# Optimization experiments

Measured on AMD Instinct MI355X. Metric: run time of the kernel, lower is better.

The kernel has to match this reference:

```python
import jax, jax.numpy as jnp
import numpy as np

G, N, E, B = 4, 50000, 800000, 32
F_IN, H, HEADS, NUM_NODES = 64, 128, 8, 50000
HD = H // HEADS
LO, HI = 50.0, 110.0


def setup_inputs() -> dict:
    key = jax.random.key(0)
    ks = jax.random.split(key, 10)
    x = jax.random.normal(ks[0], (G, N, F_IN), jnp.float32)
    edge_index = jax.random.randint(ks[1], (G, 2, E), 0, N)
    batch = jnp.sort(jax.random.randint(ks[2], (G, N), 0, B), axis=-1)
    init = lambda k, shape, fan: (jax.random.normal(k, shape, jnp.float32) / np.sqrt(fan)).astype(jnp.float32)
    W1 = init(ks[3], (F_IN, H), F_IN); b1 = jnp.zeros((H,), jnp.float32)
    W2 = init(ks[4], (H, H), H);       b2 = jnp.zeros((H,), jnp.float32)
    in_proj_w = init(ks[5], (3 * H, H), H); in_proj_b = jnp.zeros((3 * H,), jnp.float32)
    out_proj_w = init(ks[6], (H, H), H);    out_proj_b = jnp.zeros((H,), jnp.float32)
    lin_w = init(ks[7], (NUM_NODES, H), H); lin_b = jnp.zeros((NUM_NODES,), jnp.float32)
    return dict(x=x, edge_index=edge_index, batch=batch, W1=W1, b1=b1, W2=W2, b2=b2,
                in_proj_w=in_proj_w, in_proj_b=in_proj_b, out_proj_w=out_proj_w,
                out_proj_b=out_proj_b, lin_w=lin_w, lin_b=lin_b)


def _gcn(x, row, col, W, b):
    # PyG GCNConv: add self-loops, sym-normalized scatter-add aggregation.
    h = x @ W  # [N,H]
    deg = jax.ops.segment_sum(jnp.ones((E,), x.dtype), col, num_segments=N) + 1.0  # +1 self-loop
    dinv = jax.lax.rsqrt(deg)
    norm = dinv[row] * dinv[col]  # [E]
    agg = jax.ops.segment_sum(h[row] * norm[:, None], col, num_segments=N)
    agg = agg + h * (1.0 / deg)[:, None]  # self-loop message (norm = 1/deg)
    return agg + b


def _per_graph(xg, eig, bg, W1, b1, W2, b2):
    row, col = eig[0], eig[1]
    h = jax.nn.relu(_gcn(xg, row, col, W1, b1))
    h = jax.nn.relu(_gcn(h, row, col, W2, b2))
    s = jax.ops.segment_sum(h, bg, num_segments=B)  # [B,H]
    cnt = jax.ops.segment_sum(jnp.ones((N,), h.dtype), bg, num_segments=B)
    return jnp.where(cnt[:, None] > 0, s / jnp.maximum(cnt, 1.0)[:, None], 0.0)


def reference(x, edge_index, batch, W1, b1, W2, b2, in_proj_w, in_proj_b,
              out_proj_w, out_proj_b, lin_w, lin_b):
    # per-graph GCN + mean pool -> embeddings [G, B, H] (seq-first for torch MHA)
    emb = jax.vmap(_per_graph, in_axes=(0, 0, 0, None, None, None, None))(
        x, edge_index, batch, W1, b1, W2, b2)
    # torch MultiheadAttention (self-attention, seq-first)
    q = emb @ in_proj_w[:H].T + in_proj_b[:H]
    k = emb @ in_proj_w[H:2 * H].T + in_proj_b[H:2 * H]
    v = emb @ in_proj_w[2 * H:].T + in_proj_b[2 * H:]
    qh = q.reshape(G, B, HEADS, HD)
    kh = k.reshape(G, B, HEADS, HD)
    vh = v.reshape(G, B, HEADS, HD)
    scores = jnp.einsum('gbhd,kbhd->bhgk', qh, kh) / np.sqrt(HD)
    attn = jax.nn.softmax(scores, axis=-1)
    ctx = jnp.einsum('bhgk,kbhd->gbhd', attn, vh).reshape(G, B, H)
    attended = ctx @ out_proj_w.T + out_proj_b  # [G,B,H]
    pooled = attended.mean(axis=1)  # [G,H]
    out = pooled @ lin_w.T + lin_b  # [G,NUM_NODES]
    return out * (HI - LO) + LO
```

## Files before the change

kernel.cpp:

```cpp
#include <hip/hip_runtime.h>

#define Gn 4
#define Nn 50000
#define En 800000
#define Bq 32
#define F_IN 64
#define Hn 128
#define NNODES 50000
#define NBK 196
#define EB 98

using v8s = __attribute__((ext_vector_type(8))) short;
using v4f = __attribute__((ext_vector_type(4))) float;

__device__ __forceinline__ float bf2f(unsigned short u) {
    unsigned int x = ((unsigned int)u) << 16;
    float f; __builtin_memcpy(&f, &x, 4); return f;
}
__device__ __forceinline__ unsigned short f2bf(float f) {
    unsigned int x; __builtin_memcpy(&x, &f, 4);
    x = (x + 0x7fffu + ((x >> 16) & 1u)) >> 16;
    return (unsigned short)x;
}

__global__ __launch_bounds__(256) void k_btot(const int* __restrict__ ei, int* __restrict__ btot,
                                              int* __restrict__ chist) {
    __shared__ int h[NBK];
    int g = blockIdx.y;
    const int* col = ei + (size_t)g * 2 * En + En;
    for (int i = threadIdx.x; i < NBK; i += 256) h[i] = 0;
    __syncthreads();
    int e0 = blockIdx.x * 8192, e1 = min(e0 + 8192, En);
    for (int i = e0 / 4 + threadIdx.x; i < e1 / 4; i += 256) {
        int4 c = ((const int4*)col)[i];
        atomicAdd(&h[c.x >> 8], 1);
        atomicAdd(&h[c.y >> 8], 1);
        atomicAdd(&h[c.z >> 8], 1);
        atomicAdd(&h[c.w >> 8], 1);
    }
    __syncthreads();
    int* ch = chist + ((size_t)g * EB + blockIdx.x) * NBK;
    for (int i = threadIdx.x; i < NBK; i += 256) {
        int v = h[i];
        ch[i] = v;
        if (v) atomicAdd(&btot[g * NBK + i], v);
    }
}

__global__ __launch_bounds__(256) void k_bbase(const int* __restrict__ btot, int* __restrict__ bbase,
                                               int* __restrict__ bcur) {
    __shared__ int s[256];
    int g = blockIdx.x, t = threadIdx.x;
    int v = (t < NBK) ? btot[g * NBK + t] : 0;
    s[t] = v;
    __syncthreads();
    for (int d = 1; d < 256; d <<= 1) {
        int u = (t >= d) ? s[t - d] : 0;
        __syncthreads();
        s[t] += u;
        __syncthreads();
    }
    if (t < NBK) { int b = s[t] - v; bbase[g * NBK + t] = b; bcur[g * NBK + t] = b; }
}

__global__ __launch_bounds__(256) void k_bucket(const int* __restrict__ ei, int* __restrict__ bcur,
                                                unsigned int* __restrict__ pairs,
                                                const int* __restrict__ chist) {
    __shared__ int h[NBK];
    __shared__ int gbase[NBK];
    int g = blockIdx.y;
    const int* row = ei + (size_t)g * 2 * En;
    const int* col = row + En;
    unsigned int* pg = pairs + (size_t)g * En;
    const int* ch = chist + ((size_t)g * EB + blockIdx.x) * NBK;
    for (int i = threadIdx.x; i < NBK; i += 256) {
        int cnt = ch[i];
        gbase[i] = cnt ? atomicAdd(&bcur[g * NBK + i], cnt) : 0;
        h[i] = 0;
    }
    __syncthreads();
    int e0 = blockIdx.x * 8192, e1 = min(e0 + 8192, En);
    for (int i = e0 / 4 + threadIdx.x; i < e1 / 4; i += 256) {
        int4 c = ((const int4*)col)[i];
        int4 r = ((const int4*)row)[i];
        int p;
        p = gbase[c.x >> 8] + atomicAdd(&h[c.x >> 8], 1); pg[p] = ((unsigned)r.x << 16) | (unsigned)c.x;
        p = gbase[c.y >> 8] + atomicAdd(&h[c.y >> 8], 1); pg[p] = ((unsigned)r.y << 16) | (unsigned)c.y;
        p = gbase[c.z >> 8] + atomicAdd(&h[c.z >> 8], 1); pg[p] = ((unsigned)r.z << 16) | (unsigned)c.z;
        p = gbase[c.w >> 8] + atomicAdd(&h[c.w >> 8], 1); pg[p] = ((unsigned)r.w << 16) | (unsigned)c.w;
    }
}

__global__ __launch_bounds__(256) void k_fillb2(const unsigned int* __restrict__ pairs,
                                                const int* __restrict__ bbase, const int* __restrict__ btot,
                                                int* __restrict__ off, float* __restrict__ dinv,
                                                unsigned short* __restrict__ srcs) {
    __shared__ int h[256], sc[256], curL[256];
    int g = blockIdx.y, b = blockIdx.x, t = threadIdx.x;
    int beg = bbase[g * NBK + b], cnt = btot[g * NBK + b];
    const unsigned int* pg = pairs + (size_t)g * En + beg;
    unsigned short* sg = srcs + (size_t)g * En;
    h[t] = 0;
    __syncthreads();
    for (int i = t; i < cnt; i += 256) atomicAdd(&h[pg[i] & 255], 1);
    __syncthreads();
    int d = h[t];
    sc[t] = d;
    __syncthreads();
    for (int dd = 1; dd < 256; dd <<= 1) {
        int u = (t >= dd) ? sc[t - dd] : 0;
        __syncthreads();
        sc[t] += u;
        __syncthreads();
    }
    int myoff = beg + sc[t] - d;
    int node = b * 256 + t;
    if (node < Nn) {
        off[g * (Nn + 1) + node] = myoff;
        dinv[g * Nn + node] = rsqrtf((float)d + 1.0f);
    }
    if (b == NBK - 1 && t == 255) off[g * (Nn + 1) + Nn] = beg + sc[255];
    curL[t] = myoff;
    __syncthreads();
    for (int i = t; i < cnt; i += 256) {
        unsigned int pr = pg[i];
        int pos = atomicAdd(&curL[pr & 255], 1);
        sg[pos] = (unsigned short)(pr >> 16);
    }
}

__global__ __launch_bounds__(256) void k_cast(const float* __restrict__ x, const float* __restrict__ dinv,
                                              unsigned short* __restrict__ xbs) {
    int g = blockIdx.y;
    int i = blockIdx.x * 256 + threadIdx.x;
    if (i >= Nn * 16) return;
    float dc = dinv[g * Nn + (i >> 4)];
    float4 v = *(const float4*)&x[(size_t)g * Nn * 64 + i * 4];
    ushort4 u = make_ushort4(f2bf(v.x * dc), f2bf(v.y * dc), f2bf(v.z * dc), f2bf(v.w * dc));
    *(ushort4*)&xbs[(size_t)g * Nn * 64 + i * 4] = u;
}

__global__ __launch_bounds__(256) void k_agg1(const unsigned short* __restrict__ xs_, const int* __restrict__ off_,
                                              const unsigned short* __restrict__ srcs_,
                                              const float* __restrict__ dinv_, unsigned short* __restrict__ z1_) {
    int g = blockIdx.y;
    const unsigned short* xs = xs_ + (size_t)g * Nn * 64;
    const int* off = off_ + g * (Nn + 1);
    const unsigned short* srcs = srcs_ + (size_t)g * En;
    unsigned short* z1 = z1_ + (size_t)g * Nn * 64;
    int node = blockIdx.x * 8 + (threadIdx.x >> 5);
    int lane = threadIdx.x & 31;
    int sub = lane >> 3;
    int fo = lane & 7;
    int beg = off[node], end = off[node + 1];
    int d = end - beg;
    int dm1 = max(d - 1, 0);
    int nst = (d + 3) >> 2;
    float acc[8] = {};
    int sb = srcs[beg + min(sub, dm1)];
    v8s c = *(const v8s*)&xs[(long)sb * 64 + fo * 8];
    sb = srcs[beg + min(4 + sub, dm1)];
    for (int st = 0; st < nst; ++st) {
        v8s n = *(const v8s*)&xs[(long)sb * 64 + fo * 8];
        sb = srcs[beg + min((st + 2) * 4 + sub, dm1)];
        float m = (st * 4 + sub < d) ? 1.f : 0.f;
#pragma unroll
        for (int q = 0; q < 8; ++q) acc[q] += m * bf2f((unsigned short)c[q]);
        c = n;
    }
#pragma unroll
    for (int q = 0; q < 8; ++q) {
        acc[q] += __shfl_xor(acc[q], 8, 32);
        acc[q] += __shfl_xor(acc[q], 16, 32);
    }
    if (sub == 0) {
        float dc = dinv_[g * Nn + node];
        v8s ow = *(const v8s*)&xs[(long)node * 64 + fo * 8];
        ushort4 o0, o1;
        o0.x = f2bf((acc[0] + bf2f((unsigned short)ow[0])) * dc);
        o0.y = f2bf((acc[1] + bf2f((unsigned short)ow[1])) * dc);
        o0.z = f2bf((acc[2] + bf2f((unsigned short)ow[2])) * dc);
        o0.w = f2bf((acc[3] + bf2f((unsigned short)ow[3])) * dc);
        o1.x = f2bf((acc[4] + bf2f((unsigned short)ow[4])) * dc);
        o1.y = f2bf((acc[5] + bf2f((unsigned short)ow[5])) * dc);
        o1.z = f2bf((acc[6] + bf2f((unsigned short)ow[6])) * dc);
        o1.w = f2bf((acc[7] + bf2f((unsigned short)ow[7])) * dc);
        *(ushort4*)&z1[(long)node * 64 + fo * 8] = o0;
        *(ushort4*)&z1[(long)node * 64 + fo * 8 + 4] = o1;
    }
}

__global__ __launch_bounds__(256) void k_agg2(const unsigned short* __restrict__ h_, const int* __restrict__ off_,
                                              const unsigned short* __restrict__ srcs_,
                                              const float* __restrict__ dinv_, unsigned short* __restrict__ z2_) {
    int g = blockIdx.y;
    const unsigned short* h = h_ + (size_t)g * Nn * 128;
    const int* off = off_ + g * (Nn + 1);
    const unsigned short* srcs = srcs_ + (size_t)g * En;
    unsigned short* z2 = z2_ + (size_t)g * Nn * 128;
    int node = blockIdx.x * 8 + (threadIdx.x >> 5);
    int lane = threadIdx.x & 31;
    int sub = lane >> 3;
    int fo = lane & 7;
    int beg = off[node], end = off[node + 1];
    int d = end - beg;
    int dm1 = max(d - 1, 0);
    int nst = (d + 3) >> 2;
    float acc[16] = {};
    int sb = srcs[beg + min(sub, dm1)];
    const unsigned short* rp = &h[(long)sb * 128 + fo * 16];
    v8s c0 = *(const v8s*)rp;
    v8s c1 = *(const v8s*)(rp + 8);
    sb = srcs[beg + min(4 + sub, dm1)];
    for (int st = 0; st < nst; ++st) {
        const unsigned short* rpn = &h[(long)sb * 128 + fo * 16];
        v8s n0 = *(const v8s*)rpn;
        v8s n1 = *(const v8s*)(rpn + 8);
        sb = srcs[beg + min((st + 2) * 4 + sub, dm1)];
        float m = (st * 4 + sub < d) ? 1.f : 0.f;
#pragma unroll
        for (int q = 0; q < 8; ++q) acc[q] += m * bf2f((unsigned short)c0[q]);
#pragma unroll
        for (int q = 0; q < 8; ++q) acc[8 + q] += m * bf2f((unsigned short)c1[q]);
        c0 = n0; c1 = n1;
    }
#pragma unroll
    for (int q = 0; q < 16; ++q) {
        acc[q] += __shfl_xor(acc[q], 8, 32);
        acc[q] += __shfl_xor(acc[q], 16, 32);
    }
    if (sub == 0) {
        float dc = dinv_[g * Nn + node];
        const unsigned short* op = &h[(long)node * 128 + fo * 16];
        unsigned short* zp = &z2[(long)node * 128 + fo * 16];
#pragma unroll
        for (int q4 = 0; q4 < 4; ++q4) {
            ushort4 ow = *(const ushort4*)(op + q4 * 4);
            ushort4 o;
            o.x = f2bf((acc[q4 * 4 + 0] + bf2f(ow.x)) * dc);
            o.y = f2bf((acc[q4 * 4 + 1] + bf2f(ow.y)) * dc);
            o.z = f2bf((acc[q4 * 4 + 2] + bf2f(ow.z)) * dc);
            o.w = f2bf((acc[q4 * 4 + 3] + bf2f(ow.w)) * dc);
            *(ushort4*)(zp + q4 * 4) = o;
        }
    }
}

template <int K, bool SCALE>
__global__ __launch_bounds__(256) void k_mmfma(const unsigned short* __restrict__ zin_,
                                               const float* __restrict__ W, const float* __restrict__ bias,
                                               const float* __restrict__ dinv_,
                                               unsigned short* __restrict__ outp_) {
    __shared__ __align__(16) unsigned short Wt[128 * (K + 8)];
    __shared__ __align__(16) unsigned short At[32 * (K + 8)];
    int g = blockIdx.y;
    const unsigned short* zin = zin_ + (size_t)g * Nn * K;
    const float* dinv = dinv_ + g * Nn;
    unsigned short* outp = outp_ + (size_t)g * Nn * 128;
    int t = threadIdx.x;
    int base = blockIdx.x * 32;

#pragma unroll
    for (int i = 0; i < K * 128 / 256; ++i) {
        int idx = i * 256 + t;
        int k = idx >> 7, n = idx & 127;
        Wt[n * (K + 8) + k] = f2bf(W[idx]);
    }
    {
        int r = t >> 3, cb = (t & 7) * (K / 8);
        long grow = base + r;
#pragma unroll
        for (int j = 0; j < K / 32; ++j) {
            ushort4 u = make_ushort4(0, 0, 0, 0);
            if (grow < Nn) u = *(const ushort4*)&zin[grow * K + cb + j * 4];
            *(ushort4*)&At[r * (K + 8) + cb + j * 4] = u;
        }
    }
    __syncthreads();

    int w = t >> 6, lane = t & 63;
    int wm = w & 1, wn = w >> 1;
    int m = lane & 15, q = lane >> 4;
    v4f acc[4] = {};
    const unsigned short* Ap = &At[(wm * 16 + m) * (K + 8) + q * 8];
    const unsigned short* Bp = &Wt[(wn * 64 + m) * (K + 8) + q * 8];
    const int rstep = 16 * (K + 8);
#pragma unroll
    for (int ks = 0; ks < K / 32; ++ks) {
        v8s a = *(const v8s*)(Ap + ks * 32);
        v8s b0 = *(const v8s*)(Bp + 0 * rstep + ks * 32);
        v8s b1 = *(const v8s*)(Bp + 1 * rstep + ks * 32);
        v8s b2 = *(const v8s*)(Bp + 2 * rstep + ks * 32);
        v8s b3 = *(const v8s*)(Bp + 3 * rstep + ks * 32);
        acc[0] = __builtin_amdgcn_mfma_f32_16x16x32_bf16(a, b0, acc[0], 0, 0, 0);
        acc[1] = __builtin_amdgcn_mfma_f32_16x16x32_bf16(a, b1, acc[1], 0, 0, 0);
        acc[2] = __builtin_amdgcn_mfma_f32_16x16x32_bf16(a, b2, acc[2], 0, 0, 0);
        acc[3] = __builtin_amdgcn_mfma_f32_16x16x32_bf16(a, b3, acc[3], 0, 0, 0);
    }

    int col0 = wn * 64 + m;
    int rbase = base + wm * 16 + q * 4;
    float dv[4];
#pragma unroll
    for (int rg = 0; rg < 4; ++rg)
        dv[rg] = SCALE ? ((rbase + rg < Nn) ? dinv[rbase + rg] : 1.f) : 1.f;
#pragma unroll
    for (int nt = 0; nt < 4; ++nt) {
        float bc = bias[col0 + nt * 16];
#pragma unroll
        for (int rg = 0; rg < 4; ++rg) {
            int row = rbase + rg;
            if (row < Nn) {
                float o = fmaxf(acc[nt][rg] + bc, 0.f);
                outp[(long)row * 128 + col0 + nt * 16] = f2bf(o * dv[rg]);
            }
        }
    }
}

__global__ __launch_bounds__(128) void k_pool(const unsigned short* __restrict__ y_, const int* __restrict__ bat,
                                              float* __restrict__ emb_sum, float* __restrict__ cnt) {
    int g = blockIdx.y;
    const unsigned short* y = y_ + (size_t)g * Nn * 128;
    const int* batch = bat + (size_t)g * Nn;
    int f = threadIdx.x;
    int start = blockIdx.x * 64;
    int end = min(start + 64, Nn);
    if (start >= Nn) return;
    float acc = 0.f;
    int cacc = 0;
    int cur = batch[start];
    for (int i = start; i < end; ++i) {
        int b = batch[i];
        if (b != cur) {
            atomicAdd(&emb_sum[(g * Bq + cur) * Hn + f], acc);
            if (f == 0) atomicAdd(&cnt[g * Bq + cur], (float)cacc);
            acc = 0.f; cacc = 0; cur = b;
        }
        acc += bf2f(y[(long)i * Hn + f]);
        cacc++;
    }
    atomicAdd(&emb_sum[(g * Bq + cur) * Hn + f], acc);
    if (f == 0) atomicAdd(&cnt[g * Bq + cur], (float)cacc);
}

__global__ __launch_bounds__(128) void k_attn(const float* __restrict__ emb_sum, const float* __restrict__ cnt,
                                              const float* __restrict__ ipw, const float* __restrict__ ipb,
                                              const float* __restrict__ opw, const float* __restrict__ opb,
                                              float* __restrict__ pooled) {
    int b = blockIdx.x;
    int f = threadIdx.x;
    __shared__ float es[4][128], qs[4][128], ks[4][128], vs[4][128], sc[128], cx[4][128];
#pragma unroll
    for (int g = 0; g < 4; ++g) {
        float c = cnt[g * Bq + b];
        es[g][f] = (c > 0.f) ? emb_sum[(g * Bq + b) * Hn + f] / c : 0.f;
    }
    __syncthreads();
#pragma unroll
    for (int g = 0; g < 4; ++g) {
        float q = ipb[f], k = ipb[Hn + f], v = ipb[2 * Hn + f];
        for (int j = 0; j < Hn; ++j) {
            float e = es[g][j];
            q += e * ipw[f * Hn + j];
            k += e * ipw[(Hn + f) * Hn + j];
            v += e * ipw[(2 * Hn + f) * Hn + j];
        }
        qs[g][f] = q; ks[g][f] = k; vs[g][f] = v;
    }
    __syncthreads();
    {
        int h = f >> 4, g = (f >> 2) & 3, kk = f & 3;
        float s = 0.f;
        for (int d = 0; d < 16; ++d) s += qs[g][h * 16 + d] * ks[kk][h * 16 + d];
        sc[f] = s * 0.25f;
    }
    __syncthreads();
    {
        int h = f >> 4;
#pragma unroll
        for (int g = 0; g < 4; ++g) {
            int bi = h * 16 + g * 4;
            float s0 = sc[bi], s1 = sc[bi + 1], s2 = sc[bi + 2], s3 = sc[bi + 3];
            float m = fmaxf(fmaxf(s0, s1), fmaxf(s2, s3));
            float e0 = __expf(s0 - m), e1 = __expf(s1 - m), e2 = __expf(s2 - m), e3 = __expf(s3 - m);
            float rinv = 1.f / (e0 + e1 + e2 + e3);
            cx[g][f] = (e0 * vs[0][f] + e1 * vs[1][f] + e2 * vs[2][f] + e3 * vs[3][f]) * rinv;
        }
    }
    __syncthreads();
#pragma unroll
    for (int g = 0; g < 4; ++g) {
        float a = opb[f];
        for (int j = 0; j < Hn; ++j) a += cx[g][j] * opw[f * Hn + j];
        atomicAdd(&pooled[g * Hn + f], a * (1.0f / Bq));
    }
}

__global__ __launch_bounds__(256) void k_final(const float* __restrict__ pooled, const float* __restrict__ lw,
                                               const float* __restrict__ lb, float* __restrict__ out) {
    __shared__ float ps[512];
    int t = threadIdx.x;
    ps[t] = pooled[t];
    ps[t + 256] = pooled[t + 256];
    __syncthreads();
    int wave = t >> 6, lane = t & 63;
    int n = blockIdx.x * 4 + wave;
    if (n >= NNODES) return;
    float2 w = *(const float2*)&lw[(long)n * 128 + lane * 2];
    float a0 = w.x * ps[0 * 128 + lane * 2] + w.y * ps[0 * 128 + lane * 2 + 1];
    float a1 = w.x * ps[1 * 128 + lane * 2] + w.y * ps[1 * 128 + lane * 2 + 1];
    float a2 = w.x * ps[2 * 128 + lane * 2] + w.y * ps[2 * 128 + lane * 2 + 1];
    float a3 = w.x * ps[3 * 128 + lane * 2] + w.y * ps[3 * 128 + lane * 2 + 1];
#pragma unroll
    for (int off = 32; off > 0; off >>= 1) {
        a0 += __shfl_down(a0, off);
        a1 += __shfl_down(a1, off);
        a2 += __shfl_down(a2, off);
        a3 += __shfl_down(a3, off);
    }
    if (lane == 0) {
        float bn = lb[n];
        out[0 * NNODES + n] = (a0 + bn) * 60.f + 50.f;
        out[1 * NNODES + n] = (a1 + bn) * 60.f + 50.f;
        out[2 * NNODES + n] = (a2 + bn) * 60.f + 50.f;
        out[3 * NNODES + n] = (a3 + bn) * 60.f + 50.f;
    }
}

extern "C" void kernel_launch(void* const* d_in, const int* in_sizes, int n_in,
                              void* d_out, int out_size, void* d_ws, size_t ws_size,
                              hipStream_t stream) {
    const float* x   = (const float*)d_in[0];
    const int*   ei  = (const int*)d_in[1];
    const int*   bat = (const int*)d_in[2];
    const float* W1  = (const float*)d_in[3];
    const float* b1  = (const float*)d_in[4];
    const float* W2  = (const float*)d_in[5];
    const float* b2  = (const float*)d_in[6];
    const float* ipw = (const float*)d_in[7];
    const float* ipb = (const float*)d_in[8];
    const float* opw = (const float*)d_in[9];
    const float* opb = (const float*)d_in[10];
    const float* lw  = (const float*)d_in[11];
    const float* lb  = (const float*)d_in[12];
    float* out = (float*)d_out;

    char* p = (char*)d_ws;
    unsigned short* xbs = (unsigned short*)p;
    unsigned short* z1  = (unsigned short*)(p + 25600000);
    unsigned short* y1b = (unsigned short*)(p + 51200000);
    unsigned short* z2  = (unsigned short*)(p + 102400000);
    unsigned int*   pairs = (unsigned int*)(p + 102400000);
    int* chist = (int*)(p + 102400000 + (size_t)4 * En * 4);
    unsigned short* y2b = (unsigned short*)(p + 153600000);
    char* meta = p + 204800000;
    int*   off  = (int*)meta;
    float* dinv = (float*)(off + 4 * (Nn + 1));
    int*   btot  = (int*)(dinv + 4 * Nn);
    int*   bbase = btot + 4 * NBK;
    int*   bcur  = bbase + 4 * NBK;
    unsigned short* srcs = (unsigned short*)(bcur + 4 * NBK);
    float* emb    = (float*)(srcs + (size_t)4 * En);
    float* cnt    = emb + Gn * Bq * Hn;
    float* pooled = cnt + Gn * Bq;

    hipMemsetAsync(btot, 0, 4 * NBK * sizeof(int), stream);
    hipMemsetAsync(emb, 0, Gn * Bq * Hn * sizeof(float), stream);
    hipMemsetAsync(cnt, 0, Gn * Bq * sizeof(float), stream);
    hipMemsetAsync(pooled, 0, Gn * Hn * sizeof(float), stream);

    const int agGrid = (Nn + 7) / 8;
    const int mmGrid = (Nn + 31) / 32;
    const int plGrid = (Nn + 63) / 64;
    const int ctGrid = (Nn * 16 + 255) / 256;

    k_btot<<<dim3(EB, Gn), 256, 0, stream>>>(ei, btot, chist);
    k_bbase<<<Gn, 256, 0, stream>>>(btot, bbase, bcur);
    k_bucket<<<dim3(EB, Gn), 256, 0, stream>>>(ei, bcur, pairs, chist);
    k_fillb2<<<dim3(NBK, Gn), 256, 0, stream>>>(pairs, bbase, btot, off, dinv, srcs);

    k_cast<<<dim3(ctGrid, Gn), 256, 0, stream>>>(x, dinv, xbs);
    k_agg1<<<dim3(agGrid, Gn), 256, 0, stream>>>(xbs, off, srcs, dinv, z1);
    k_mmfma<64, true><<<dim3(mmGrid, Gn), 256, 0, stream>>>(z1, W1, b1, dinv, y1b);
    k_agg2<<<dim3(agGrid, Gn), 256, 0, stream>>>(y1b, off, srcs, dinv, z2);
    k_mmfma<128, false><<<dim3(mmGrid, Gn), 256, 0, stream>>>(z2, W2, b2, dinv, y2b);
    k_pool<<<dim3(plGrid, Gn), 128, 0, stream>>>(y2b, bat, emb, cnt);

    k_attn<<<Bq, 128, 0, stream>>>(emb, cnt, ipw, ipb, opw, opb, pooled);
    k_final<<<(NNODES + 3) / 4, 256, 0, stream>>>(pooled, lw, lb, out);
}
```

Before: 526.7 us.

## Use full wavefront per node in aggregation with packed bf16 unpacking

The two neighbour-aggregation kernels now assign one 64-lane wavefront per node instead of 32 lanes, so eight neighbours are gathered per step instead of four, and the grid doubles to match. The bf16-to-float conversion reads packed 32-bit words and unpacks two values at a time into float2 vectors, which may map to packed FMA instructions. Index arithmetic moves from 64-bit to 32-bit unsigned. The cost is an extra shuffle-reduction stage, and low-degree nodes leave more lanes idle.

New measurement: 578.0 us. 1.1x slower.

```diff
diff --git a/kernel.cpp b/kernel.cpp
--- a/kernel.cpp
+++ b/kernel.cpp
@@ -12,6 +12,7 @@
 
 using v8s = __attribute__((ext_vector_type(8))) short;
 using v4f = __attribute__((ext_vector_type(4))) float;
+using v2f = __attribute__((ext_vector_type(2))) float;
 
 __device__ __forceinline__ float bf2f(unsigned short u) {
     unsigned int x = ((unsigned int)u) << 16;
@@ -21,6 +22,14 @@
     unsigned int x; __builtin_memcpy(&x, &f, 4);
     x = (x + 0x7fffu + ((x >> 16) & 1u)) >> 16;
     return (unsigned short)x;
+}
+__device__ __forceinline__ v2f up2(unsigned int w) {
+    unsigned int lo = w << 16, hi = w & 0xffff0000u;
+    float flo, fhi;
+    __builtin_memcpy(&flo, &lo, 4);
+    __builtin_memcpy(&fhi, &hi, 4);
+    v2f v = {flo, fhi};
+    return v;
 }
 
 __global__ __launch_bounds__(256) void k_btot(const int* __restrict__ ei, int* __restrict__ btot,
@@ -148,45 +157,52 @@
     const int* off = off_ + g * (Nn + 1);
     const unsigned short* srcs = srcs_ + (size_t)g * En;
     unsigned short* z1 = z1_ + (size_t)g * Nn * 64;
-    int node = blockIdx.x * 8 + (threadIdx.x >> 5);
-    int lane = threadIdx.x & 31;
+    int node = blockIdx.x * 4 + (threadIdx.x >> 6);
+    int lane = threadIdx.x & 63;
     int sub = lane >> 3;
     int fo = lane & 7;
     int beg = off[node], end = off[node + 1];
     int d = end - beg;
     int dm1 = max(d - 1, 0);
-    int nst = (d + 3) >> 2;
-    float acc[8] = {};
+    int nst = (d + 7) >> 3;
+    v2f acc[4] = {};
     int sb = srcs[beg + min(sub, dm1)];
-    v8s c = *(const v8s*)&xs[(long)sb * 64 + fo * 8];
-    sb = srcs[beg + min(4 + sub, dm1)];
+    uint4 c = *(const uint4*)&xs[(unsigned)sb * 64 + fo * 8];
+    sb = srcs[beg + min(8 + sub, dm1)];
     for (int st = 0; st < nst; ++st) {
-        v8s n = *(const v8s*)&xs[(long)sb * 64 + fo * 8];
-        sb = srcs[beg + min((st + 2) * 4 + sub, dm1)];
-        float m = (st * 4 + sub < d) ? 1.f : 0.f;
-#pragma unroll
-        for (int q = 0; q < 8; ++q) acc[q] += m * bf2f((unsigned short)c[q]);
+        uint4 n = *(const uint4*)&xs[(unsigned)sb * 64 + fo * 8];
+        sb = srcs[beg + min((st + 2) * 8 + sub, dm1)];
+        float m = (st * 8 + sub < d) ? 1.f : 0.f;
+        v2f m2 = {m, m};
+        acc[0] += m2 * up2(c.x);
+        acc[1] += m2 * up2(c.y);
+        acc[2] += m2 * up2(c.z);
+        acc[3] += m2 * up2(c.w);
         c = n;
     }
 #pragma unroll
-    for (int q = 0; q < 8; ++q) {
-        acc[q] += __shfl_xor(acc[q], 8, 32);
-        acc[q] += __shfl_xor(acc[q], 16, 32);
+    for (int p = 0; p < 4; ++p) {
+        float ax = acc[p].x, ay = acc[p].y;
+        ax += __shfl_xor(ax, 8, 64);  ay += __shfl_xor(ay, 8, 64);
+        ax += __shfl_xor(ax, 16, 64); ay += __shfl_xor(ay, 16, 64);
+        ax += __shfl_xor(ax, 32, 64); ay += __shfl_xor(ay, 32, 64);
+        acc[p].x = ax; acc[p].y = ay;
     }
     if (sub == 0) {
         float dc = dinv_[g * Nn + node];
-        v8s ow = *(const v8s*)&xs[(long)node * 64 + fo * 8];
+        uint4 ow = *(const uint4*)&xs[(unsigned)node * 64 + fo * 8];
+        v2f s0 = up2(ow.x), s1 = up2(ow.y), s2 = up2(ow.z), s3 = up2(ow.w);
         ushort4 o0, o1;
-        o0.x = f2bf((acc[0] + bf2f((unsigned short)ow[0])) * dc);
-        o0.y = f2bf((acc[1] + bf2f((unsigned short)ow[1])) * dc);
-        o0.z = f2bf((acc[2] + bf2f((unsigned short)ow[2])) * dc);
-        o0.w = f2bf((acc[3] + bf2f((unsigned short)ow[3])) * dc);
-        o1.x = f2bf((acc[4] + bf2f((unsigned short)ow[4])) * dc);
-        o1.y = f2bf((acc[5] + bf2f((unsigned short)ow[5])) * dc);
-        o1.z = f2bf((acc[6] + bf2f((unsigned short)ow[6])) * dc);
-        o1.w = f2bf((acc[7] + bf2f((unsigned short)ow[7])) * dc);
-        *(ushort4*)&z1[(long)node * 64 + fo * 8] = o0;
-        *(ushort4*)&z1[(long)node * 64 + fo * 8 + 4] = o1;
+        o0.x = f2bf((acc[0].x + s0.x) * dc);
+        o0.y = f2bf((acc[0].y + s0.y) * dc);
+        o0.z = f2bf((acc[1].x + s1.x) * dc);
+        o0.w = f2bf((acc[1].y + s1.y) * dc);
+        o1.x = f2bf((acc[2].x + s2.x) * dc);
+        o1.y = f2bf((acc[2].y + s2.y) * dc);
+        o1.z = f2bf((acc[3].x + s3.x) * dc);
+        o1.w = f2bf((acc[3].y + s3.y) * dc);
+        *(ushort4*)&z1[(unsigned)node * 64 + fo * 8] = o0;
+        *(ushort4*)&z1[(unsigned)node * 64 + fo * 8 + 4] = o1;
     }
 }
 
@@ -198,50 +214,62 @@
     const int* off = off_ + g * (Nn + 1);
     const unsigned short* srcs = srcs_ + (size_t)g * En;
     unsigned short* z2 = z2_ + (size_t)g * Nn * 128;
-    int node = blockIdx.x * 8 + (threadIdx.x >> 5);
-    int lane = threadIdx.x & 31;
+    int node = blockIdx.x * 4 + (threadIdx.x >> 6);
+    int lane = threadIdx.x & 63;
     int sub = lane >> 3;
     int fo = lane & 7;
     int beg = off[node], end = off[node + 1];
     int d = end - beg;
     int dm1 = max(d - 1, 0);
-    int nst = (d + 3) >> 2;
-    float acc[16] = {};
+    int nst = (d + 7) >> 3;
+    v2f acc[8] = {};
     int sb = srcs[beg + min(sub, dm1)];
-    const unsigned short* rp = &h[(long)sb * 128 + fo * 16];
-    v8s c0 = *(const v8s*)rp;
-    v8s c1 = *(const v8s*)(rp + 8);
-    sb = srcs[beg + min(4 + sub, dm1)];
+    const uint4* rp = (const uint4*)&h[(unsigned)sb * 128 + fo * 16];
+    uint4 c0 = rp[0], c1 = rp[1];
+    sb = srcs[beg + min(8 + sub, dm1)];
     for (int st = 0; st < nst; ++st) {
-        const unsigned short* rpn = &h[(long)sb * 128 + fo * 16];
-        v8s n0 = *(const v8s*)rpn;
-        v8s n1 = *(const v8s*)(rpn + 8);
-        sb = srcs[beg + min((st + 2) * 4 + sub, dm1)];
-        float m = (st * 4 + sub < d) ? 1.f : 0.f;
-#pragma unroll
-        for (int q = 0; q < 8; ++q) acc[q] += m * bf2f((unsigned short)c0[q]);
-#pragma unroll
-        for (int q = 0; q < 8; ++q) acc[8 + q] += m * bf2f((unsigned short)c1[q]);
+        const uint4* rpn = (const uint4*)&h[(unsigned)sb * 128 + fo * 16];
+        uint4 n0 = rpn[0], n1 = rpn[1];
+        sb = srcs[beg + min((st + 2) * 8 + sub, dm1)];
+        float m = (st * 8 + sub < d) ? 1.f : 0.f;
+        v2f m2 = {m, m};
+        acc[0] += m2 * up2(c0.x);
+        acc[1] += m2 * up2(c0.y);
+        acc[2] += m2 * up2(c0.z);
+        acc[3] += m2 * up2(c0.w);
+        acc[4] += m2 * up2(c1.x);
+        acc[5] += m2 * up2(c1.y);
+        acc[6] += m2 * up2(c1.z);
+        acc[7] += m2 * up2(c1.w);
         c0 = n0; c1 = n1;
     }
 #pragma unroll
-    for (int q = 0; q < 16; ++q) {
-        acc[q] += __shfl_xor(acc[q], 8, 32);
-        acc[q] += __shfl_xor(acc[q], 16, 32);
+    for (int p = 0; p < 8; ++p) {
+        float ax = acc[p].x, ay = acc[p].y;
+        ax += __shfl_xor(ax, 8, 64);  ay += __shfl_xor(ay, 8, 64);
+        ax += __shfl_xor(ax, 16, 64); ay += __shfl_xor(ay, 16, 64);
+        ax += __shfl_xor(ax, 32, 64); ay += __shfl_xor(ay, 32, 64);
+        acc[p].x = ax; acc[p].y = ay;
     }
     if (sub == 0) {
         float dc = dinv_[g * Nn + node];
-        const unsigned short* op = &h[(long)node * 128 + fo * 16];
-        unsigned short* zp = &z2[(long)node * 128 + fo * 16];
-#pragma unroll
-        for (int q4 = 0; q4 < 4; ++q4) {
-            ushort4 ow = *(const ushort4*)(op + q4 * 4);
-            ushort4 o;
-            o.x = f2bf((acc[q4 * 4 + 0] + bf2f(ow.x)) * dc);
-            o.y = f2bf((acc[q4 * 4 + 1] + bf2f(ow.y)) * dc);
-            o.z = f2bf((acc[q4 * 4 + 2] + bf2f(ow.z)) * dc);
-            o.w = f2bf((acc[q4 * 4 + 3] + bf2f(ow.w)) * dc);
-            *(ushort4*)(zp + q4 * 4) = o;
+        const unsigned short* op = &h[(unsigned)node * 128 + fo * 16];
+        unsigned short* zp = &z2[(unsigned)node * 128 + fo * 16];
+#pragma unroll
+        for (int p4 = 0; p4 < 2; ++p4) {
+            uint4 ow = *(const uint4*)(op + p4 * 8);
+            v2f s0 = up2(ow.x), s1 = up2(ow.y), s2 = up2(ow.z), s3 = up2(ow.w);
+            ushort4 oa, ob;
+            oa.x = f2bf((acc[p4 * 4 + 0].x + s0.x) * dc);
+            oa.y = f2bf((acc[p4 * 4 + 0].y + s0.y) * dc);
+            oa.z = f2bf((acc[p4 * 4 + 1].x + s1.x) * dc);
+            oa.w = f2bf((acc[p4 * 4 + 1].y + s1.y) * dc);
+            ob.x = f2bf((acc[p4 * 4 + 2].x + s2.x) * dc);
+            ob.y = f2bf((acc[p4 * 4 + 2].y + s2.y) * dc);
+            ob.z = f2bf((acc[p4 * 4 + 3].x + s3.x) * dc);
+            ob.w = f2bf((acc[p4 * 4 + 3].y + s3.y) * dc);
+            *(ushort4*)(zp + p4 * 8) = oa;
+            *(ushort4*)(zp + p4 * 8 + 4) = ob;
         }
     }
 }
@@ -470,7 +498,7 @@
     hipMemsetAsync(cnt, 0, Gn * Bq * sizeof(float), stream);
     hipMemsetAsync(pooled, 0, Gn * Hn * sizeof(float), stream);
 
-    const int agGrid = (Nn + 7) / 8;
+    const int agGrid = (Nn + 3) / 4;
     const int mmGrid = (Nn + 31) / 32;
     const int plGrid = (Nn + 63) / 64;
     const int ctGrid = (Nn * 16 + 255) / 256;
```
